# Optimization experiments

Hardware: AMD Instinct MI355X
Metric: run time of the kernel (lower is better)

## Reference

```python
import jax, jax.numpy as jnp
import numpy as np

# ---- module config (init_kwargs) ----
LAT = 512          # lat_size
OUT_SIZE = 32768   # out_size
NF = 128           # n_filter
NCALLS = 4         # n_calls
CUBE = int(np.ceil(OUT_SIZE ** (1.0 / 3.0)))  # 32
CF = 3             # SinSobel c_factor for dim=3 (one sin-sobel gradient per axis)
FIN, FH, FO = NF * CF, NF, NF
# hypernet output: w_in(FH,FIN)+b_in(FH)+w_mid(FH,FH)+b_mid(FH)+w_out(FO,FH)+b_out(FO)+w_short(FO,FIN)+b_short(FO)
KTOT = FH * FIN + FH + FH * FH + FH + FO * FH + FO + FO * FIN + FO  # 131584
EPS = 1e-5


def _inorm(x):
    # InstanceNorm3d, affine=False: normalize each (b, c) over D,H,W
    m = x.mean(axis=(2, 3, 4), keepdims=True)
    v = x.var(axis=(2, 3, 4), keepdims=True)
    return (x - m) * jax.lax.rsqrt(v + EPS)


def _sobel_kernel():
    # SinSobel: fixed sinusoidal sobel gradient along each of the 3 axes
    g = jnp.sin(jnp.linspace(-1.0, 1.0, 3) * (jnp.pi / 2.0))  # [-1, 0, 1]
    kx = jnp.broadcast_to(g[:, None, None], (3, 3, 3))
    ky = jnp.broadcast_to(g[None, :, None], (3, 3, 3))
    kz = jnp.broadcast_to(g[None, None, :], (3, 3, 3))
    base = jnp.stack([kx, ky, kz])[:, None]          # (3, 1, 3, 3, 3)
    return jnp.tile(base, (NF, 1, 1, 1, 1))           # (NF*3, 1, 3, 3, 3) depthwise


def setup_inputs() -> dict:
    key = jax.random.key(0)
    k1, k2, k3, k4 = jax.random.split(key, 4)
    B = 4
    lat = jax.random.normal(k1, (B, LAT), jnp.float32)
    seed = jax.random.normal(k2, (1, NF, CUBE, CUBE, CUBE), jnp.float32)
    W_k = jax.random.normal(k3, (LAT, KTOT), jnp.float32) * 0.02  # hypernet weight
    b_k = jax.random.normal(k4, (KTOT,), jnp.float32) * 0.02      # hypernet bias
    return {"lat": lat, "seed": seed, "W_k": W_k, "b_k": b_k}


def _forward(lat, seed, W_k, b_k):
    B = lat.shape[0]
    V = CUBE ** 3
    # hypernetwork: per-sample dynamic 1x1x1 conv weights
    ks = lat @ W_k + b_k  # (B, KTOT)
    idx = [0]
    def take(n, shape):
        w = ks[:, idx[0]:idx[0] + n].reshape((B,) + shape)
        idx[0] += n
        return w
    w_in = take(FH * FIN, (FH, FIN)); b_in = take(FH, (FH, 1))
    w_mid = take(FH * FH, (FH, FH));  b_mid = take(FH, (FH, 1))
    w_out = take(FO * FH, (FO, FH));  b_out = take(FO, (FO, 1))
    w_sh = take(FO * FIN, (FO, FIN)); b_sh = take(FO, (FO, 1))

    sob = _sobel_kernel()
    out = _inorm(jnp.tile(seed, (B, 1, 1, 1, 1)))  # seed_norm

    def body(out, _):
        # fixed depthwise sin-sobel conv3d: (B,NF,S,S,S) -> (B,3*NF,S,S,S)
        y = jax.lax.conv_general_dilated(
            out, sob, (1, 1, 1), 'SAME',
            dimension_numbers=('NCDHW', 'OIDHW', 'NCDHW'),
            feature_group_count=NF)
        y = _inorm(y).reshape(B, FIN, V)
        # DynaResidualBlock: per-sample 1x1x1 convs == batched matmuls
        h = jax.nn.relu(jnp.einsum('bcv,bhc->bhv', y, w_in) + b_in)
        h = jax.nn.relu(jnp.einsum('bcv,bhc->bhv', h, w_mid) + b_mid)
        h = jnp.einsum('bcv,boc->bov', h, w_out) + b_out
        s = jnp.einsum('bcv,boc->bov', y, w_sh) + b_sh
        y = (h + s).reshape(B, NF, CUBE, CUBE, CUBE)
        return out + 0.1 * y, None

    out, _ = jax.lax.scan(body, out, None, length=NCALLS)
    return out.mean(1).reshape(B, -1)[:, :OUT_SIZE]


def reference(lat, seed, W_k, b_k):
    return _forward(lat, seed, W_k, b_k)
```

## Files before the change

### kernel.cpp

```cpp
#include <hip/hip_runtime.h>
#include <cstdint>
#include <cstddef>

#define BB 4
#define LATN 512
#define NFC 128
#define FIN 384
#define KTOT 131584
#define VV 32768
#define NCALLS 4

typedef unsigned short u16;
typedef unsigned int u32;
typedef __bf16 v8bf __attribute__((ext_vector_type(8)));
typedef float v4f __attribute__((ext_vector_type(4)));

__device__ inline u16 f2bf(float f) {
  u32 u = __builtin_bit_cast(u32, f);
  u += 0x7fffu + ((u >> 16) & 1u);
  return (u16)(u >> 16);
}

__global__ __launch_bounds__(256) void k_hyper(const float* __restrict__ lat,
    const float* __restrict__ Wk, const float* __restrict__ bk,
    float* __restrict__ ks, u16* __restrict__ wbf)
{
  __shared__ float lats[BB * LATN];
  int tid = threadIdx.x;
  for (int i = tid; i < BB * LATN; i += 256) lats[i] = lat[i];
  __syncthreads();
  int k = blockIdx.x * 256 + tid;
  float a0 = 0.f, a1 = 0.f, a2 = 0.f, a3 = 0.f;
  for (int l = 0; l < LATN; ++l) {
    float w = Wk[(size_t)l * KTOT + k];
    a0 = fmaf(w, lats[l], a0);
    a1 = fmaf(w, lats[LATN + l], a1);
    a2 = fmaf(w, lats[2 * LATN + l], a2);
    a3 = fmaf(w, lats[3 * LATN + l], a3);
  }
  float bv = bk[k];
  a0 += bv; a1 += bv; a2 += bv; a3 += bv;
  ks[k] = a0; ks[KTOT + k] = a1; ks[2 * (size_t)KTOT + k] = a2; ks[3 * (size_t)KTOT + k] = a3;
  wbf[k] = f2bf(a0); wbf[KTOT + k] = f2bf(a1);
  wbf[2 * (size_t)KTOT + k] = f2bf(a2); wbf[3 * (size_t)KTOT + k] = f2bf(a3);
}

__global__ __launch_bounds__(256) void k_seednorm(const float* __restrict__ seed,
                                                  float* __restrict__ outb)
{
  int c = blockIdx.x;
  const float* s = seed + (size_t)c * VV;
  int tid = threadIdx.x;
  float sum = 0.f, sq = 0.f;
  for (int v = tid; v < VV; v += 256) { float x = s[v]; sum += x; sq = fmaf(x, x, sq); }
  #pragma unroll
  for (int off = 32; off; off >>= 1) { sum += __shfl_down(sum, off); sq += __shfl_down(sq, off); }
  __shared__ float r0[4], r1[4]; __shared__ float mb, rb;
  int wid = tid >> 6, lid = tid & 63;
  if (lid == 0) { r0[wid] = sum; r1[wid] = sq; }
  __syncthreads();
  if (tid == 0) {
    float st = r0[0] + r0[1] + r0[2] + r0[3];
    float qt = r1[0] + r1[1] + r1[2] + r1[3];
    float m = st / (float)VV;
    float var = qt / (float)VV - m * m;
    mb = m; rb = rsqrtf(var + 1e-5f);
  }
  __syncthreads();
  float m = mb, r = rb;
  for (int v = tid; v < VV; v += 256) {
    float x = (s[v] - m) * r;
    outb[(size_t)(0 * NFC + c) * VV + v] = x;
    outb[(size_t)(1 * NFC + c) * VV + v] = x;
    outb[(size_t)(2 * NFC + c) * VV + v] = x;
    outb[(size_t)(3 * NFC + c) * VV + v] = x;
  }
}

__global__ __launch_bounds__(256) void k_conv(const float* __restrict__ outb,
    u16* __restrict__ yb, float* __restrict__ stats)
{
  int bc = blockIdx.x;
  const float* x = outb + (size_t)bc * VV;
  int b = bc >> 7, c = bc & 127;
  u16* y0 = yb + (size_t)(b * FIN + 3 * c) * VV;
  float s0 = 0, q0 = 0, s1 = 0, q1 = 0, s2 = 0, q2 = 0;
  for (int rr = threadIdx.x; rr < 1024; rr += 256) {
    int d = rr >> 5, h = rr & 31;
    float g1[32], g2[32], g3[32];
    #pragma unroll
    for (int i = 0; i < 32; ++i) { g1[i] = 0.f; g2[i] = 0.f; g3[i] = 0.f; }
    for (int dd = -1; dd <= 1; ++dd) {
      int D = d + dd; if ((unsigned)D >= 32u) continue;
      float fd = (float)dd;
      for (int dh = -1; dh <= 1; ++dh) {
        int H = h + dh; if ((unsigned)H >= 32u) continue;
        float fh = (float)dh;
        const float4* rp = (const float4*)(x + (D << 10) + (H << 5));
        #pragma unroll
        for (int w4 = 0; w4 < 8; ++w4) {
          float4 v = rp[w4];
          int base = w4 * 4;
          g1[base + 0] = fmaf(fd, v.x, g1[base + 0]); g2[base + 0] = fmaf(fh, v.x, g2[base + 0]); g3[base + 0] += v.x;
          g1[base + 1] = fmaf(fd, v.y, g1[base + 1]); g2[base + 1] = fmaf(fh, v.y, g2[base + 1]); g3[base + 1] += v.y;
          g1[base + 2] = fmaf(fd, v.z, g1[base + 2]); g2[base + 2] = fmaf(fh, v.z, g2[base + 2]); g3[base + 2] += v.z;
          g1[base + 3] = fmaf(fd, v.w, g1[base + 3]); g2[base + 3] = fmaf(fh, v.w, g2[base + 3]); g3[base + 3] += v.w;
        }
      }
    }
    int rowoff = rr << 5;
    u16 pa[32], pe[32], pz[32];
    #pragma unroll
    for (int w = 0; w < 32; ++w) {
      float a = g1[w] + (w > 0 ? g1[w - 1] : 0.f) + (w < 31 ? g1[w + 1] : 0.f);
      float e = g2[w] + (w > 0 ? g2[w - 1] : 0.f) + (w < 31 ? g2[w + 1] : 0.f);
      float z = (w < 31 ? g3[w + 1] : 0.f) - (w > 0 ? g3[w - 1] : 0.f);
      s0 += a; q0 = fmaf(a, a, q0);
      s1 += e; q1 = fmaf(e, e, q1);
      s2 += z; q2 = fmaf(z, z, q2);
      pa[w] = f2bf(a); pe[w] = f2bf(e); pz[w] = f2bf(z);
    }
    #pragma unroll
    for (int w8 = 0; w8 < 4; ++w8) {
      *(uint4*)(y0 + rowoff + w8 * 8) = *(uint4*)(pa + w8 * 8);
      *(uint4*)(y0 + (size_t)VV + rowoff + w8 * 8) = *(uint4*)(pe + w8 * 8);
      *(uint4*)(y0 + 2 * (size_t)VV + rowoff + w8 * 8) = *(uint4*)(pz + w8 * 8);
    }
  }
  float vals[6] = { s0, q0, s1, q1, s2, q2 };
  __shared__ float red[6][4];
  int wid = threadIdx.x >> 6, lid = threadIdx.x & 63;
  #pragma unroll
  for (int t = 0; t < 6; ++t) {
    float v = vals[t];
    #pragma unroll
    for (int off = 32; off; off >>= 1) v += __shfl_down(v, off);
    if (lid == 0) red[t][wid] = v;
  }
  __syncthreads();
  if (threadIdx.x == 0) {
    #pragma unroll
    for (int a = 0; a < 3; ++a) {
      float st = red[2 * a][0] + red[2 * a][1] + red[2 * a][2] + red[2 * a][3];
      float qt = red[2 * a + 1][0] + red[2 * a + 1][1] + red[2 * a + 1][2] + red[2 * a + 1][3];
      float m = st / (float)VV;
      float var = qt / (float)VV - m * m;
      float rs = rsqrtf(var + 1e-5f);
      int oc = b * FIN + 3 * c + a;
      stats[2 * oc] = m; stats[2 * oc + 1] = rs;
    }
  }
}

__global__ __launch_bounds__(256) void k_trans(const u16* __restrict__ yb,
                                               u16* __restrict__ yt)
{
  int b = blockIdx.x >> 7;
  int vtile = blockIdx.x & 127;
  int tid = threadIdx.x;
  int wave = tid >> 6, lane = tid & 63;
  int vi = lane >> 3, ki = lane & 7;
  int v0 = vtile * 256 + wave * 64 + vi * 8;
  const u16* src = yb + (size_t)b * FIN * VV;
  u16* dst = yt + (size_t)b * VV * FIN;
  union U { uint4 q; u16 s[8]; };
  #pragma unroll
  for (int kb = 0; kb < 6; ++kb) {
    int k0 = kb * 64 + ki * 8;
    U r[8], c[8];
    #pragma unroll
    for (int i = 0; i < 8; ++i)
      r[i].q = *(const uint4*)(src + (size_t)(k0 + i) * VV + v0);
    #pragma unroll
    for (int j = 0; j < 8; ++j) {
      #pragma unroll
      for (int i = 0; i < 8; ++i) c[j].s[i] = r[i].s[j];
    }
    #pragma unroll
    for (int j = 0; j < 8; ++j)
      *(uint4*)(dst + (size_t)(v0 + j) * FIN + k0) = c[j].q;
  }
}

__global__ __launch_bounds__(128) void k_prep(const float* __restrict__ ks,
    const float* __restrict__ stats, u16* __restrict__ wbf, float* __restrict__ badj)
{
  int b = blockIdx.x >> 1, which = blockIdx.x & 1;
  int h = threadIdx.x;
  const float* ksb = ks + (size_t)b * KTOT;
  const float2* st = (const float2*)(stats + b * FIN * 2);
  int woff = which ? 82304 : 0;
  const float* ws = ksb + woff + h * FIN;
  u16* wd = wbf + (size_t)b * KTOT + woff + h * FIN;
  float accm = 0.f;
  for (int cc = 0; cc < FIN; ++cc) {
    float2 mr = st[cc];
    float sw = ws[cc] * mr.y;
    wd[cc] = f2bf(sw);
    accm = fmaf(sw, mr.x, accm);
  }
  int boff = which ? 131456 : 49152;
  badj[b * 256 + which * 128 + h] = ksb[boff + h] - accm;
}

#define HPAD 136

__global__ __launch_bounds__(256, 2) void k_mlp(
    const u16* __restrict__ wbf, const float* __restrict__ ks,
    const float* __restrict__ badj, const u16* __restrict__ yt,
    float* __restrict__ outb)
{
  __shared__ u16 hs[128 * HPAD];
  int b = blockIdx.y;
  int tid = threadIdx.x;
  int lane = tid & 63, wave = tid >> 6;
  int ln = lane & 15, quad = lane >> 4;
  int n0 = blockIdx.x * 128;
  const u16* wb = wbf + (size_t)b * KTOT;
  const float* ksb = ks + (size_t)b * KTOT;
  const float* bj = badj + b * 256;

  v4f acc1[8][2], acc3[8][2];
  #pragma unroll
  for (int i = 0; i < 8; ++i)
    for (int j = 0; j < 2; ++j) { acc1[i][j] = (v4f){0,0,0,0}; acc3[i][j] = (v4f){0,0,0,0}; }

  const u16* x0 = yt + ((size_t)b * VV + n0 + wave * 32 + ln) * FIN + quad * 8;
  const u16* x1 = x0 + (size_t)16 * FIN;
  const u16* api = wb + 0     + (size_t)ln * FIN + quad * 8;
  const u16* aps = wb + 82304 + (size_t)ln * FIN + quad * 8;
  v8bf bf0 = *(const v8bf*)x0;
  v8bf bf1 = *(const v8bf*)x1;
  #pragma unroll 2
  for (int c = 0; c < 12; ++c) {
    int k0 = c * 32;
    v8bf nb0 = bf0, nb1 = bf1;
    if (c < 11) {
      nb0 = *(const v8bf*)(x0 + k0 + 32);
      nb1 = *(const v8bf*)(x1 + k0 + 32);
    }
    #pragma unroll
    for (int mt = 0; mt < 8; ++mt) {
      v8bf ai = *(const v8bf*)(api + (size_t)mt * 16 * FIN + k0);
      acc1[mt][0] = __builtin_amdgcn_mfma_f32_16x16x32_bf16(ai, bf0, acc1[mt][0], 0, 0, 0);
      acc1[mt][1] = __builtin_amdgcn_mfma_f32_16x16x32_bf16(ai, bf1, acc1[mt][1], 0, 0, 0);
    }
    #pragma unroll
    for (int mt = 0; mt < 8; ++mt) {
      v8bf as = *(const v8bf*)(aps + (size_t)mt * 16 * FIN + k0);
      acc3[mt][0] = __builtin_amdgcn_mfma_f32_16x16x32_bf16(as, bf0, acc3[mt][0], 0, 0, 0);
      acc3[mt][1] = __builtin_amdgcn_mfma_f32_16x16x32_bf16(as, bf1, acc3[mt][1], 0, 0, 0);
    }
    bf0 = nb0; bf1 = nb1;
  }
  #pragma unroll
  for (int nt = 0; nt < 2; ++nt) {
    int nl = wave * 32 + nt * 16 + ln;
    #pragma unroll
    for (int mt = 0; mt < 8; ++mt) {
      int m = mt * 16 + quad * 4;
      ushort4 pk;
      pk.x = f2bf(fmaxf(acc1[mt][nt][0] + bj[m + 0], 0.f));
      pk.y = f2bf(fmaxf(acc1[mt][nt][1] + bj[m + 1], 0.f));
      pk.z = f2bf(fmaxf(acc1[mt][nt][2] + bj[m + 2], 0.f));
      pk.w = f2bf(fmaxf(acc1[mt][nt][3] + bj[m + 3], 0.f));
      *(ushort4*)&hs[nl * HPAD + m] = pk;
    }
  }
  __syncthreads();

  v4f acc2[8][2];
  #pragma unroll
  for (int i = 0; i < 8; ++i)
    for (int j = 0; j < 2; ++j) acc2[i][j] = (v4f){0,0,0,0};
  const u16* apm = wb + 49280 + (size_t)ln * 128 + quad * 8;
  #pragma unroll
  for (int c = 0; c < 4; ++c) {
    int k0 = c * 32;
    v8bf bv0 = *(const v8bf*)&hs[(wave * 32 + ln) * HPAD + quad * 8 + k0];
    v8bf bv1 = *(const v8bf*)&hs[(wave * 32 + 16 + ln) * HPAD + quad * 8 + k0];
    #pragma unroll
    for (int mt = 0; mt < 8; ++mt) {
      v8bf am = *(const v8bf*)(apm + (size_t)mt * 16 * 128 + k0);
      acc2[mt][0] = __builtin_amdgcn_mfma_f32_16x16x32_bf16(am, bv0, acc2[mt][0], 0, 0, 0);
      acc2[mt][1] = __builtin_amdgcn_mfma_f32_16x16x32_bf16(am, bv1, acc2[mt][1], 0, 0, 0);
    }
  }
  __syncthreads();
  #pragma unroll
  for (int nt = 0; nt < 2; ++nt) {
    int nl = wave * 32 + nt * 16 + ln;
    #pragma unroll
    for (int mt = 0; mt < 8; ++mt) {
      int m = mt * 16 + quad * 4;
      ushort4 pk;
      pk.x = f2bf(fmaxf(acc2[mt][nt][0] + ksb[65664 + m + 0], 0.f));
      pk.y = f2bf(fmaxf(acc2[mt][nt][1] + ksb[65664 + m + 1], 0.f));
      pk.z = f2bf(fmaxf(acc2[mt][nt][2] + ksb[65664 + m + 2], 0.f));
      pk.w = f2bf(fmaxf(acc2[mt][nt][3] + ksb[65664 + m + 3], 0.f));
      *(ushort4*)&hs[nl * HPAD + m] = pk;
    }
  }
  __syncthreads();

  const u16* apo = wb + 65792 + (size_t)ln * 128 + quad * 8;
  #pragma unroll
  for (int c = 0; c < 4; ++c) {
    int k0 = c * 32;
    v8bf bv0 = *(const v8bf*)&hs[(wave * 32 + ln) * HPAD + quad * 8 + k0];
    v8bf bv1 = *(const v8bf*)&hs[(wave * 32 + 16 + ln) * HPAD + quad * 8 + k0];
    #pragma unroll
    for (int mt = 0; mt < 8; ++mt) {
      v8bf ao = *(const v8bf*)(apo + (size_t)mt * 16 * 128 + k0);
      acc3[mt][0] = __builtin_amdgcn_mfma_f32_16x16x32_bf16(ao, bv0, acc3[mt][0], 0, 0, 0);
      acc3[mt][1] = __builtin_amdgcn_mfma_f32_16x16x32_bf16(ao, bv1, acc3[mt][1], 0, 0, 0);
    }
  }

  #pragma unroll
  for (int nt = 0; nt < 2; ++nt) {
    int n = n0 + wave * 32 + nt * 16 + ln;
    #pragma unroll
    for (int mt = 0; mt < 8; ++mt) {
      #pragma unroll
      for (int r = 0; r < 4; ++r) {
        int m = mt * 16 + quad * 4 + r;
        float t = acc3[mt][nt][r] + ksb[82176 + m] + bj[128 + m];
        outb[(size_t)(b * 128 + m) * VV + n] += 0.1f * t;
      }
    }
  }
}

__global__ __launch_bounds__(256) void k_mean(const float* __restrict__ outb,
                                              float* __restrict__ dout)
{
  int idx = blockIdx.x * 256 + threadIdx.x;
  int b = idx >> 15, v = idx & (VV - 1);
  const float* p = outb + (size_t)b * NFC * VV + v;
  float s = 0.f;
  for (int c = 0; c < NFC; ++c) s += p[(size_t)c * VV];
  dout[idx] = s * (1.0f / (float)NFC);
}

extern "C" void kernel_launch(void* const* d_in, const int* in_sizes, int n_in,
                              void* d_out, int out_size, void* d_ws, size_t ws_size,
                              hipStream_t stream)
{
  const float* lat  = (const float*)d_in[0];
  const float* seed = (const float*)d_in[1];
  const float* Wk   = (const float*)d_in[2];
  const float* bk   = (const float*)d_in[3];

  char* p = (char*)d_ws;
  float* ks    = (float*)p; p += (size_t)BB * KTOT * 4;
  u16*   wbf   = (u16*)p;   p += (size_t)BB * KTOT * 2;
  float* badj  = (float*)p; p += (size_t)BB * 256 * 4;
  float* stats = (float*)p; p += (size_t)BB * FIN * 2 * 4;
  float* outb  = (float*)p; p += (size_t)BB * NFC * VV * 4;
  u16*   yb    = (u16*)p;   p += (size_t)BB * FIN * VV * 2;
  u16*   yt    = (u16*)p;   p += (size_t)BB * VV * FIN * 2;
  (void)ws_size; (void)in_sizes; (void)n_in; (void)out_size;

  k_hyper<<<dim3(KTOT / 256), 256, 0, stream>>>(lat, Wk, bk, ks, wbf);
  k_seednorm<<<dim3(NFC), 256, 0, stream>>>(seed, outb);

  for (int t = 0; t < NCALLS; ++t) {
    k_conv<<<dim3(BB * NFC), 256, 0, stream>>>(outb, yb, stats);
    k_trans<<<dim3(512), 256, 0, stream>>>(yb, yt);
    k_prep<<<dim3(8), 128, 0, stream>>>(ks, stats, wbf, badj);
    k_mlp<<<dim3(VV / 128, BB), 256, 0, stream>>>(wbf, ks, badj, yt, outb);
  }
  k_mean<<<dim3((BB * VV) / 256), 256, 0, stream>>>(outb, (float*)d_out);
}
```

Before: 1.664 ms.

## Halve MLP tile to 64 voxels per block and software-pipeline weight loads

Each k_mlp block now covers 64 voxels instead of 128, so each wave handles one 16-column tile instead of two. This halves accumulator registers and shared memory, and launch bounds rise to 3 blocks per SM. The first GEMM loop now prefetches the activation B-fragments three k-steps ahead and the w_in A-fragments one step ahead. The cost is that weights are reused across half as many columns, so weight traffic from global/L2 per voxel doubles.

```diff
diff --git a/kernel.cpp b/kernel.cpp
--- a/kernel.cpp
+++ b/kernel.cpp
@@ -205,101 +205,92 @@
 
 #define HPAD 136
 
-__global__ __launch_bounds__(256, 2) void k_mlp(
+__global__ __launch_bounds__(256, 3) void k_mlp(
     const u16* __restrict__ wbf, const float* __restrict__ ks,
     const float* __restrict__ badj, const u16* __restrict__ yt,
     float* __restrict__ outb)
 {
-  __shared__ u16 hs[128 * HPAD];
+  __shared__ u16 hs[64 * HPAD];
   int b = blockIdx.y;
   int tid = threadIdx.x;
   int lane = tid & 63, wave = tid >> 6;
   int ln = lane & 15, quad = lane >> 4;
-  int n0 = blockIdx.x * 128;
+  int n0 = blockIdx.x * 64;
+  int nw = wave * 16;
   const u16* wb = wbf + (size_t)b * KTOT;
   const float* ksb = ks + (size_t)b * KTOT;
   const float* bj = badj + b * 256;
 
-  v4f acc1[8][2], acc3[8][2];
-  #pragma unroll
-  for (int i = 0; i < 8; ++i)
-    for (int j = 0; j < 2; ++j) { acc1[i][j] = (v4f){0,0,0,0}; acc3[i][j] = (v4f){0,0,0,0}; }
-
-  const u16* x0 = yt + ((size_t)b * VV + n0 + wave * 32 + ln) * FIN + quad * 8;
-  const u16* x1 = x0 + (size_t)16 * FIN;
+  v4f acc1[8], acc3[8];
+  #pragma unroll
+  for (int i = 0; i < 8; ++i) { acc1[i] = (v4f){0,0,0,0}; acc3[i] = (v4f){0,0,0,0}; }
+
+  const u16* x0  = yt + ((size_t)b * VV + n0 + nw + ln) * FIN + quad * 8;
   const u16* api = wb + 0     + (size_t)ln * FIN + quad * 8;
   const u16* aps = wb + 82304 + (size_t)ln * FIN + quad * 8;
-  v8bf bf0 = *(const v8bf*)x0;
-  v8bf bf1 = *(const v8bf*)x1;
-  #pragma unroll 2
+
+  v8bf bufB[3];
+  bufB[0] = *(const v8bf*)(x0);
+  bufB[1] = *(const v8bf*)(x0 + 32);
+  bufB[2] = *(const v8bf*)(x0 + 64);
+  v8bf ai[8];
+  #pragma unroll
+  for (int mt = 0; mt < 8; ++mt) ai[mt] = *(const v8bf*)(api + (size_t)mt * 16 * FIN);
+
+  #pragma unroll
   for (int c = 0; c < 12; ++c) {
     int k0 = c * 32;
-    v8bf nb0 = bf0, nb1 = bf1;
-    if (c < 11) {
-      nb0 = *(const v8bf*)(x0 + k0 + 32);
-      nb1 = *(const v8bf*)(x1 + k0 + 32);
-    }
+    v8bf bv = bufB[c % 3];
+    if (c + 3 < 12) bufB[c % 3] = *(const v8bf*)(x0 + k0 + 96);
     #pragma unroll
     for (int mt = 0; mt < 8; ++mt) {
-      v8bf ai = *(const v8bf*)(api + (size_t)mt * 16 * FIN + k0);
-      acc1[mt][0] = __builtin_amdgcn_mfma_f32_16x16x32_bf16(ai, bf0, acc1[mt][0], 0, 0, 0);
-      acc1[mt][1] = __builtin_amdgcn_mfma_f32_16x16x32_bf16(ai, bf1, acc1[mt][1], 0, 0, 0);
+      acc1[mt] = __builtin_amdgcn_mfma_f32_16x16x32_bf16(ai[mt], bv, acc1[mt], 0, 0, 0);
+      if (c + 1 < 12)
+        ai[mt] = *(const v8bf*)(api + (size_t)mt * 16 * FIN + k0 + 32);
     }
     #pragma unroll
     for (int mt = 0; mt < 8; ++mt) {
       v8bf as = *(const v8bf*)(aps + (size_t)mt * 16 * FIN + k0);
-      acc3[mt][0] = __builtin_amdgcn_mfma_f32_16x16x32_bf16(as, bf0, acc3[mt][0], 0, 0, 0);
-      acc3[mt][1] = __builtin_amdgcn_mfma_f32_16x16x32_bf16(as, bf1, acc3[mt][1], 0, 0, 0);
-    }
-    bf0 = nb0; bf1 = nb1;
-  }
-  #pragma unroll
-  for (int nt = 0; nt < 2; ++nt) {
-    int nl = wave * 32 + nt * 16 + ln;
-    #pragma unroll
-    for (int mt = 0; mt < 8; ++mt) {
-      int m = mt * 16 + quad * 4;
-      ushort4 pk;
-      pk.x = f2bf(fmaxf(acc1[mt][nt][0] + bj[m + 0], 0.f));
-      pk.y = f2bf(fmaxf(acc1[mt][nt][1] + bj[m + 1], 0.f));
-      pk.z = f2bf(fmaxf(acc1[mt][nt][2] + bj[m + 2], 0.f));
-      pk.w = f2bf(fmaxf(acc1[mt][nt][3] + bj[m + 3], 0.f));
-      *(ushort4*)&hs[nl * HPAD + m] = pk;
-    }
-  }
-  __syncthreads();
-
-  v4f acc2[8][2];
-  #pragma unroll
-  for (int i = 0; i < 8; ++i)
-    for (int j = 0; j < 2; ++j) acc2[i][j] = (v4f){0,0,0,0};
+      acc3[mt] = __builtin_amdgcn_mfma_f32_16x16x32_bf16(as, bv, acc3[mt], 0, 0, 0);
+    }
+  }
+
+  #pragma unroll
+  for (int mt = 0; mt < 8; ++mt) {
+    int m = mt * 16 + quad * 4;
+    ushort4 pk;
+    pk.x = f2bf(fmaxf(acc1[mt][0] + bj[m + 0], 0.f));
+    pk.y = f2bf(fmaxf(acc1[mt][1] + bj[m + 1], 0.f));
+    pk.z = f2bf(fmaxf(acc1[mt][2] + bj[m + 2], 0.f));
+    pk.w = f2bf(fmaxf(acc1[mt][3] + bj[m + 3], 0.f));
+    *(ushort4*)&hs[(nw + ln) * HPAD + m] = pk;
+  }
+  __syncthreads();
+
+  v4f acc2[8];
+  #pragma unroll
+  for (int i = 0; i < 8; ++i) acc2[i] = (v4f){0,0,0,0};
   const u16* apm = wb + 49280 + (size_t)ln * 128 + quad * 8;
   #pragma unroll
   for (int c = 0; c < 4; ++c) {
     int k0 = c * 32;
-    v8bf bv0 = *(const v8bf*)&hs[(wave * 32 + ln) * HPAD + quad * 8 + k0];
-    v8bf bv1 = *(const v8bf*)&hs[(wave * 32 + 16 + ln) * HPAD + quad * 8 + k0];
+    v8bf bv = *(const v8bf*)&hs[(nw + ln) * HPAD + quad * 8 + k0];
     #pragma unroll
     for (int mt = 0; mt < 8; ++mt) {
       v8bf am = *(const v8bf*)(apm + (size_t)mt * 16 * 128 + k0);
-      acc2[mt][0] = __builtin_amdgcn_mfma_f32_16x16x32_bf16(am, bv0, acc2[mt][0], 0, 0, 0);
-      acc2[mt][1] = __builtin_amdgcn_mfma_f32_16x16x32_bf16(am, bv1, acc2[mt][1], 0, 0, 0);
-    }
-  }
-  __syncthreads();
-  #pragma unroll
-  for (int nt = 0; nt < 2; ++nt) {
-    int nl = wave * 32 + nt * 16 + ln;
-    #pragma unroll
-    for (int mt = 0; mt < 8; ++mt) {
-      int m = mt * 16 + quad * 4;
-      ushort4 pk;
-      pk.x = f2bf(fmaxf(acc2[mt][nt][0] + ksb[65664 + m + 0], 0.f));
-      pk.y = f2bf(fmaxf(acc2[mt][nt][1] + ksb[65664 + m + 1], 0.f));
-      pk.z = f2bf(fmaxf(acc2[mt][nt][2] + ksb[65664 + m + 2], 0.f));
-      pk.w = f2bf(fmaxf(acc2[mt][nt][3] + ksb[65664 + m + 3], 0.f));
-      *(ushort4*)&hs[nl * HPAD + m] = pk;
-    }
+      acc2[mt] = __builtin_amdgcn_mfma_f32_16x16x32_bf16(am, bv, acc2[mt], 0, 0, 0);
+    }
+  }
+  __syncthreads();
+  #pragma unroll
+  for (int mt = 0; mt < 8; ++mt) {
+    int m = mt * 16 + quad * 4;
+    ushort4 pk;
+    pk.x = f2bf(fmaxf(acc2[mt][0] + ksb[65664 + m + 0], 0.f));
+    pk.y = f2bf(fmaxf(acc2[mt][1] + ksb[65664 + m + 1], 0.f));
+    pk.z = f2bf(fmaxf(acc2[mt][2] + ksb[65664 + m + 2], 0.f));
+    pk.w = f2bf(fmaxf(acc2[mt][3] + ksb[65664 + m + 3], 0.f));
+    *(ushort4*)&hs[(nw + ln) * HPAD + m] = pk;
   }
   __syncthreads();
 
@@ -307,27 +298,22 @@
   #pragma unroll
   for (int c = 0; c < 4; ++c) {
     int k0 = c * 32;
-    v8bf bv0 = *(const v8bf*)&hs[(wave * 32 + ln) * HPAD + quad * 8 + k0];
-    v8bf bv1 = *(const v8bf*)&hs[(wave * 32 + 16 + ln) * HPAD + quad * 8 + k0];
+    v8bf bv = *(const v8bf*)&hs[(nw + ln) * HPAD + quad * 8 + k0];
     #pragma unroll
     for (int mt = 0; mt < 8; ++mt) {
       v8bf ao = *(const v8bf*)(apo + (size_t)mt * 16 * 128 + k0);
-      acc3[mt][0] = __builtin_amdgcn_mfma_f32_16x16x32_bf16(ao, bv0, acc3[mt][0], 0, 0, 0);
-      acc3[mt][1] = __builtin_amdgcn_mfma_f32_16x16x32_bf16(ao, bv1, acc3[mt][1], 0, 0, 0);
-    }
-  }
-
-  #pragma unroll
-  for (int nt = 0; nt < 2; ++nt) {
-    int n = n0 + wave * 32 + nt * 16 + ln;
-    #pragma unroll
-    for (int mt = 0; mt < 8; ++mt) {
-      #pragma unroll
-      for (int r = 0; r < 4; ++r) {
-        int m = mt * 16 + quad * 4 + r;
-        float t = acc3[mt][nt][r] + ksb[82176 + m] + bj[128 + m];
-        outb[(size_t)(b * 128 + m) * VV + n] += 0.1f * t;
-      }
+      acc3[mt] = __builtin_amdgcn_mfma_f32_16x16x32_bf16(ao, bv, acc3[mt], 0, 0, 0);
+    }
+  }
+
+  int n = n0 + nw + ln;
+  #pragma unroll
+  for (int mt = 0; mt < 8; ++mt) {
+    #pragma unroll
+    for (int r = 0; r < 4; ++r) {
+      int m = mt * 16 + quad * 4 + r;
+      float t = acc3[mt][r] + ksb[82176 + m] + bj[128 + m];
+      outb[(size_t)(b * 128 + m) * VV + n] += 0.1f * t;
     }
   }
 }
@@ -369,7 +355,7 @@
     k_conv<<<dim3(BB * NFC), 256, 0, stream>>>(outb, yb, stats);
     k_trans<<<dim3(512), 256, 0, stream>>>(yb, yt);
     k_prep<<<dim3(8), 128, 0, stream>>>(ks, stats, wbf, badj);
-    k_mlp<<<dim3(VV / 128, BB), 256, 0, stream>>>(wbf, ks, badj, yt, outb);
+    k_mlp<<<dim3(VV / 64, BB), 256, 0, stream>>>(wbf, ks, badj, yt, outb);
   }
   k_mean<<<dim3((BB * VV) / 256), 256, 0, stream>>>(outb, (float*)d_out);
 }
```

Result: slower. 2.166 ms (+30.2%).

## Stage MLP weight tiles into LDS via async global_load_lds double buffering

Applied to the files above, without the earlier changes.

The k_mlp kernel previously read every per-sample weight fragment straight from global memory inside the MFMA loops. Now the w_in, w_mid and w_out tiles are copied into a double-buffered LDS area with global_load_lds while the current tile is used. The shortcut weights are prefetched into registers one step ahead, and the activation loads get a two-deep register prefetch. This aims to hide global load latency behind MFMA work, at the cost of extra barriers per K step, more LDS and more register pressure, which may reduce occupancy.

```diff
diff --git a/kernel.cpp b/kernel.cpp
--- a/kernel.cpp
+++ b/kernel.cpp
@@ -19,6 +19,12 @@
   u32 u = __builtin_bit_cast(u32, f);
   u += 0x7fffu + ((u >> 16) & 1u);
   return (u16)(u >> 16);
+}
+
+__device__ inline void gll16(const u16* g, u16* l) {
+  __builtin_amdgcn_global_load_lds(
+      (const __attribute__((address_space(1))) u32*)g,
+      (__attribute__((address_space(3))) u32*)l, 16, 0, 0);
 }
 
 __global__ __launch_bounds__(256) void k_hyper(const float* __restrict__ lat,
@@ -205,12 +211,26 @@
 
 #define HPAD 136
 
+__device__ inline void stage_w(const u16* __restrict__ src, int rowstride, int c,
+                               u16* dst, int wave, int lane)
+{
+  #pragma unroll
+  for (int i = 0; i < 2; ++i) {
+    int r = i * 4 + wave;
+    int m = r * 16 + (lane >> 2);
+    int q = lane & 3;
+    gll16(src + (size_t)m * rowstride + c * 32 + q * 8,
+          dst + r * 512);
+  }
+}
+
 __global__ __launch_bounds__(256, 2) void k_mlp(
     const u16* __restrict__ wbf, const float* __restrict__ ks,
     const float* __restrict__ badj, const u16* __restrict__ yt,
     float* __restrict__ outb)
 {
   __shared__ u16 hs[128 * HPAD];
+  __shared__ u16 AB[2][4096];
   int b = blockIdx.y;
   int tid = threadIdx.x;
   int lane = tid & 63, wave = tid >> 6;
@@ -225,34 +245,44 @@
   for (int i = 0; i < 8; ++i)
     for (int j = 0; j < 2; ++j) { acc1[i][j] = (v4f){0,0,0,0}; acc3[i][j] = (v4f){0,0,0,0}; }
 
-  const u16* x0 = yt + ((size_t)b * VV + n0 + wave * 32 + ln) * FIN + quad * 8;
-  const u16* x1 = x0 + (size_t)16 * FIN;
-  const u16* api = wb + 0     + (size_t)ln * FIN + quad * 8;
+  stage_w(wb + 0, FIN, 0, AB[0], wave, lane);
+
+  const u16* x0  = yt + ((size_t)b * VV + n0 + wave * 32 + ln) * FIN + quad * 8;
+  const u16* x1  = x0 + (size_t)16 * FIN;
   const u16* aps = wb + 82304 + (size_t)ln * FIN + quad * 8;
-  v8bf bf0 = *(const v8bf*)x0;
-  v8bf bf1 = *(const v8bf*)x1;
-  #pragma unroll 2
+  v8bf as_r[8];
+  #pragma unroll
+  for (int mt = 0; mt < 8; ++mt) as_r[mt] = *(const v8bf*)(aps + (size_t)mt * 16 * FIN);
+  v8bf bA0 = *(const v8bf*)(x0),      bB0 = *(const v8bf*)(x1);
+  v8bf bA1 = *(const v8bf*)(x0 + 32), bB1 = *(const v8bf*)(x1 + 32);
+  __syncthreads();
+
+  #pragma unroll
   for (int c = 0; c < 12; ++c) {
-    int k0 = c * 32;
-    v8bf nb0 = bf0, nb1 = bf1;
-    if (c < 11) {
-      nb0 = *(const v8bf*)(x0 + k0 + 32);
-      nb1 = *(const v8bf*)(x1 + k0 + 32);
-    }
-    #pragma unroll
-    for (int mt = 0; mt < 8; ++mt) {
-      v8bf ai = *(const v8bf*)(api + (size_t)mt * 16 * FIN + k0);
-      acc1[mt][0] = __builtin_amdgcn_mfma_f32_16x16x32_bf16(ai, bf0, acc1[mt][0], 0, 0, 0);
-      acc1[mt][1] = __builtin_amdgcn_mfma_f32_16x16x32_bf16(ai, bf1, acc1[mt][1], 0, 0, 0);
-    }
-    #pragma unroll
-    for (int mt = 0; mt < 8; ++mt) {
-      v8bf as = *(const v8bf*)(aps + (size_t)mt * 16 * FIN + k0);
-      acc3[mt][0] = __builtin_amdgcn_mfma_f32_16x16x32_bf16(as, bf0, acc3[mt][0], 0, 0, 0);
-      acc3[mt][1] = __builtin_amdgcn_mfma_f32_16x16x32_bf16(as, bf1, acc3[mt][1], 0, 0, 0);
-    }
-    bf0 = nb0; bf1 = nb1;
-  }
+    if (c + 1 < 12) stage_w(wb + 0, FIN, c + 1, AB[(c + 1) & 1], wave, lane);
+    v8bf b0 = (c & 1) ? bA1 : bA0;
+    v8bf b1 = (c & 1) ? bB1 : bB0;
+    if (c + 2 < 12) {
+      if (c & 1) { bA1 = *(const v8bf*)(x0 + (c + 2) * 32); bB1 = *(const v8bf*)(x1 + (c + 2) * 32); }
+      else       { bA0 = *(const v8bf*)(x0 + (c + 2) * 32); bB0 = *(const v8bf*)(x1 + (c + 2) * 32); }
+    }
+    const u16* bufc = AB[c & 1];
+    #pragma unroll
+    for (int mt = 0; mt < 8; ++mt) {
+      v8bf ai = *(const v8bf*)&bufc[(mt * 16 + ln) * 32 + quad * 8];
+      acc1[mt][0] = __builtin_amdgcn_mfma_f32_16x16x32_bf16(ai, b0, acc1[mt][0], 0, 0, 0);
+      acc1[mt][1] = __builtin_amdgcn_mfma_f32_16x16x32_bf16(ai, b1, acc1[mt][1], 0, 0, 0);
+    }
+    #pragma unroll
+    for (int mt = 0; mt < 8; ++mt) {
+      v8bf av = as_r[mt];
+      if (c + 1 < 12) as_r[mt] = *(const v8bf*)(aps + (size_t)mt * 16 * FIN + (c + 1) * 32);
+      acc3[mt][0] = __builtin_amdgcn_mfma_f32_16x16x32_bf16(av, b0, acc3[mt][0], 0, 0, 0);
+      acc3[mt][1] = __builtin_amdgcn_mfma_f32_16x16x32_bf16(av, b1, acc3[mt][1], 0, 0, 0);
+    }
+    __syncthreads();
+  }
+
   #pragma unroll
   for (int nt = 0; nt < 2; ++nt) {
     int nl = wave * 32 + nt * 16 + ln;
@@ -267,26 +297,29 @@
       *(ushort4*)&hs[nl * HPAD + m] = pk;
     }
   }
+  stage_w(wb + 49280, 128, 0, AB[0], wave, lane);
   __syncthreads();
 
   v4f acc2[8][2];
   #pragma unroll
   for (int i = 0; i < 8; ++i)
     for (int j = 0; j < 2; ++j) acc2[i][j] = (v4f){0,0,0,0};
-  const u16* apm = wb + 49280 + (size_t)ln * 128 + quad * 8;
   #pragma unroll
   for (int c = 0; c < 4; ++c) {
+    if (c + 1 < 4) stage_w(wb + 49280, 128, c + 1, AB[(c + 1) & 1], wave, lane);
     int k0 = c * 32;
     v8bf bv0 = *(const v8bf*)&hs[(wave * 32 + ln) * HPAD + quad * 8 + k0];
     v8bf bv1 = *(const v8bf*)&hs[(wave * 32 + 16 + ln) * HPAD + quad * 8 + k0];
-    #pragma unroll
-    for (int mt = 0; mt < 8; ++mt) {
-      v8bf am = *(const v8bf*)(apm + (size_t)mt * 16 * 128 + k0);
+    const u16* bufc = AB[c & 1];
+    #pragma unroll
+    for (int mt = 0; mt < 8; ++mt) {
+      v8bf am = *(const v8bf*)&bufc[(mt * 16 + ln) * 32 + quad * 8];
       acc2[mt][0] = __builtin_amdgcn_mfma_f32_16x16x32_bf16(am, bv0, acc2[mt][0], 0, 0, 0);
       acc2[mt][1] = __builtin_amdgcn_mfma_f32_16x16x32_bf16(am, bv1, acc2[mt][1], 0, 0, 0);
     }
-  }
-  __syncthreads();
+    __syncthreads();
+  }
+
   #pragma unroll
   for (int nt = 0; nt < 2; ++nt) {
     int nl = wave * 32 + nt * 16 + ln;
@@ -301,20 +334,23 @@
       *(ushort4*)&hs[nl * HPAD + m] = pk;
     }
   }
-  __syncthreads();
-
-  const u16* apo = wb + 65792 + (size_t)ln * 128 + quad * 8;
+  stage_w(wb + 65792, 128, 0, AB[0], wave, lane);
+  __syncthreads();
+
   #pragma unroll
   for (int c = 0; c < 4; ++c) {
+    if (c + 1 < 4) stage_w(wb + 65792, 128, c + 1, AB[(c + 1) & 1], wave, lane);
     int k0 = c * 32;
     v8bf bv0 = *(const v8bf*)&hs[(wave * 32 + ln) * HPAD + quad * 8 + k0];
     v8bf bv1 = *(const v8bf*)&hs[(wave * 32 + 16 + ln) * HPAD + quad * 8 + k0];
-    #pragma unroll
-    for (int mt = 0; mt < 8; ++mt) {
-      v8bf ao = *(const v8bf*)(apo + (size_t)mt * 16 * 128 + k0);
+    const u16* bufc = AB[c & 1];
+    #pragma unroll
+    for (int mt = 0; mt < 8; ++mt) {
+      v8bf ao = *(const v8bf*)&bufc[(mt * 16 + ln) * 32 + quad * 8];
       acc3[mt][0] = __builtin_amdgcn_mfma_f32_16x16x32_bf16(ao, bv0, acc3[mt][0], 0, 0, 0);
       acc3[mt][1] = __builtin_amdgcn_mfma_f32_16x16x32_bf16(ao, bv1, acc3[mt][1], 0, 0, 0);
     }
+    if (c + 1 < 4) __syncthreads();
   }
 
   #pragma unroll
```

New measurement: 1.605 ms. -3.5%, faster.
